# Kernel tuning notes

Hardware: AMD Instinct MI355X
Metric: run time of the kernel (lower is better)

## Reference

```python
import jax, jax.numpy as jnp
import numpy as np

B, NPG, D, E = 64, 1024, 128, 524288
N = B * NPG
K1, K2, K3 = 820, 656, 525  # ceil(0.8*1024), ceil(0.8*820), ceil(0.8*656)
VOCAB = 100000
EPS = 1e-5


def setup_inputs() -> dict:
    key = jax.random.key(0)
    ks = jax.random.split(key, 16)
    epg = E // B
    off = jnp.repeat(jnp.arange(B, dtype=jnp.int32) * NPG, epg)
    src = jax.random.randint(ks[0], (E,), 0, NPG, dtype=jnp.int32) + off
    dst = jax.random.randint(ks[1], (E,), 0, NPG, dtype=jnp.int32) + off
    edge_index = jnp.stack([src, dst])  # [2, E], within-graph edges
    node_idx = jax.random.randint(ks[2], (N, 1), 0, VOCAB, dtype=jnp.int32)
    def lin(k, o, i):
        return jax.random.normal(k, (o, i), jnp.float32) / np.sqrt(i).astype(np.float32)
    return dict(
        node_idx=node_idx, edge_index=edge_index,
        emb=jax.random.normal(ks[3], (VOCAB, D), jnp.float32),
        w1l=lin(ks[4], 128, D), b1l=jnp.zeros(128, jnp.float32), w1r=lin(ks[5], 128, D),
        pool_w=jax.random.normal(ks[6], (128,), jnp.float32) / np.float32(np.sqrt(128)),
        w2l=lin(ks[7], 128, 128), b2l=jnp.zeros(128, jnp.float32), w2r=lin(ks[8], 128, 128),
        fc1_w=lin(ks[9], 128, 256), fc1_b=jnp.zeros(128, jnp.float32),
        bn1_g=jnp.ones(128, jnp.float32), bn1_b=jnp.zeros(128, jnp.float32),
        fc2_w=lin(ks[10], 64, 128), fc2_b=jnp.zeros(64, jnp.float32),
        bn2_g=jnp.ones(64, jnp.float32), bn2_b=jnp.zeros(64, jnp.float32),
        lin_w=lin(ks[11], 1, 64), lin_b=jnp.zeros(1, jnp.float32),
    )


def _sage(x, src, dst, em, wl, bl, wr):
    # PyG SAGEConv: lin_l(mean_{j->i} x_j) + lin_r(x_i); em masks dropped edges
    n = x.shape[0]
    s = jax.ops.segment_sum(x[src] * em[:, None], dst, num_segments=n)
    c = jax.ops.segment_sum(em, dst, num_segments=n)
    mean = s / jnp.maximum(c, 1.0)[:, None]
    return mean @ wl.T + bl + x @ wr.T


def _topk(x, src, dst, em, w, k):
    # PyG TopKPooling: score = x.w/||w||, per-graph top-k, gate by tanh(score)
    n = x.shape[0]
    npg = n // B
    score = (x @ w) / jnp.linalg.norm(w)
    vals, idx = jax.lax.top_k(score.reshape(B, npg), k)  # [B,k]
    perm = (idx + (jnp.arange(B, dtype=idx.dtype) * npg)[:, None]).reshape(-1)
    xn = x[perm] * jnp.tanh(vals).reshape(-1)[:, None]
    new_id = jnp.full((n,), -1, jnp.int32).at[perm].set(jnp.arange(B * k, dtype=jnp.int32))
    ns, nd = new_id[src], new_id[dst]
    em2 = em * (ns >= 0) * (nd >= 0)  # keep only edges with both endpoints kept
    return xn, jnp.maximum(ns, 0), jnp.maximum(nd, 0), em2


def _readout(x, k):
    # global_max_pool || global_mean_pool (graphs are contiguous, size k)
    xr = x.reshape(B, k, -1)
    return jnp.concatenate([xr.max(axis=1), xr.mean(axis=1)], axis=1)


def _bn(x, g, b):
    m = x.mean(0)
    v = jnp.mean((x - m) ** 2, axis=0)  # biased var, as in BatchNorm1d training
    return (x - m) / jnp.sqrt(v + EPS) * g + b


def reference(node_idx, edge_index, emb, w1l, b1l, w1r, pool_w,
              w2l, b2l, w2r, fc1_w, fc1_b, bn1_g, bn1_b,
              fc2_w, fc2_b, bn2_g, bn2_b, lin_w, lin_b):
    src, dst = edge_index[0], edge_index[1]
    em = jnp.ones((E,), jnp.float32)
    x = emb[node_idx[:, 0]]                                   # [N,128]
    x = jax.nn.relu(_sage(x, src, dst, em, w1l, b1l, w1r))
    x, src, dst, em = _topk(x, src, dst, em, pool_w, K1)
    x1 = _readout(x, K1)
    x = jax.nn.relu(_sage(x, src, dst, em, w2l, b2l, w2r))
    x, src, dst, em = _topk(x, src, dst, em, pool_w, K2)
    x2 = _readout(x, K2)
    x = jax.nn.relu(_sage(x, src, dst, em, w2l, b2l, w2r))
    x, src, dst, em = _topk(x, src, dst, em, pool_w, K3)
    x3 = _readout(x, K3)
    h = x1 + x2 + x3                                          # [B,256]
    h = jax.nn.relu(_bn(h @ fc1_w.T + fc1_b, bn1_g, bn1_b))
    h = jax.nn.relu(_bn(h @ fc2_w.T + fc2_b, bn2_g, bn2_b))
    # dropout is identity in eval mode
    return jax.nn.sigmoid(h @ lin_w.T + lin_b)[:, 0]          # [B]
```

## Files before the change

### kernel.cpp

```cpp
#include <hip/hip_runtime.h>
#include <hip/hip_bf16.h>
#include <cstdint>
#include <cstddef>

#define NGRAPH 64
#define NPG0   1024
#define NNODE  65536
#define NEDGE  524288
#define EPG    8192
#define DIM    128
#define RCHUNK 16

typedef __attribute__((ext_vector_type(8))) short short8v;
typedef __attribute__((ext_vector_type(4))) float f32x4;

__device__ __forceinline__ unsigned bf16rne(float f) {
  unsigned u = __float_as_uint(f);
  return (u + 0x7FFFu + ((u >> 16) & 1u)) >> 16;
}

__global__ __launch_bounds__(256) void k_gather(const float* __restrict__ emb,
    const int* __restrict__ nid, float* __restrict__ x)
{
  int tid = blockIdx.x * 256 + threadIdx.x;
  int i = tid >> 5, lane = tid & 31;
  int row = nid[i];
  ((float4*)(x + (size_t)i * DIM))[lane] =
      ((const float4*)(emb + (size_t)row * DIM))[lane];
}

__global__ __launch_bounds__(64) void k_norm(const float* __restrict__ pw,
    float* __restrict__ inv_norm)
{
  int t = threadIdx.x;
  float a = pw[t], b = pw[t + 64];
  float v = a * a + b * b;
  for (int off = 32; off; off >>= 1) v += __shfl_xor(v, off);
  if (t == 0) *inv_norm = 1.0f / sqrtf(v);
}

__global__ __launch_bounds__(256) void k_prep_wfrag(
    const float* __restrict__ w1l, const float* __restrict__ w1r,
    const float* __restrict__ w2l, const float* __restrict__ w2r,
    short* __restrict__ whiF, short* __restrict__ wloF)
{
  int id = blockIdx.x * 256 + threadIdx.x;
  int set = id >> 15;
  int r = id & 32767;
  int j  = r & 7;
  int l  = (r >> 3) & 63;
  int nt = (r >> 9) & 7;
  int kk = r >> 12;
  int k = kk * 32 + ((l >> 4) & 3) * 8 + j;
  int n = nt * 16 + (l & 15);
  const float* wl = set ? w2l : w1l;
  const float* wr = set ? w2r : w1r;
  float w = (k < 128) ? wl[n * 128 + k] : wr[n * 128 + (k - 128)];
  unsigned hb = bf16rne(w);
  float hif = __uint_as_float(hb << 16);
  unsigned lb = bf16rne(w - hif);
  whiF[id] = (short)hb;
  wloF[id] = (short)lb;
}

__global__ __launch_bounds__(1024) void k_csr0(const int* __restrict__ ei,
    int* __restrict__ off_g, int* __restrict__ elist_g, float* __restrict__ c_out)
{
  __shared__ int cnt[1024];
  __shared__ int cur[1024];
  __shared__ int wsum[16];
  const int t = threadIdx.x, g = blockIdx.x;
  const int nodeBase = g * NPG0;
  const int e0 = g * EPG;
  cnt[t] = 0;
  __syncthreads();
  int sv8[8], dl8[8];
  #pragma unroll
  for (int i = 0; i < 8; ++i) {
    int e = e0 + t + i * 1024;
    sv8[i] = ei[e];
    dl8[i] = ei[NEDGE + e] - nodeBase;
    atomicAdd(&cnt[dl8[i]], 1);
  }
  __syncthreads();
  const int lane = t & 63, w = t >> 6;
  int cv = cnt[t];
  int x = cv;
  #pragma unroll
  for (int off = 1; off < 64; off <<= 1) {
    int y = __shfl_up(x, off);
    if (lane >= off) x += y;
  }
  if (lane == 63) wsum[w] = x;
  __syncthreads();
  if (t < 16) {
    int v = wsum[t];
    #pragma unroll
    for (int off2 = 1; off2 < 16; off2 <<= 1) {
      int y = __shfl_up(v, off2);
      if (t >= off2) v += y;
    }
    wsum[t] = v;
  }
  __syncthreads();
  int incl = x + (w ? wsum[w - 1] : 0);
  int excl = incl - cv;
  cur[t] = excl;
  int* offp = off_g + g * 1025;
  offp[t] = excl;
  if (t == 1023) offp[1024] = incl;
  c_out[nodeBase + t] = (float)cv;
  __syncthreads();
  int* elp = elist_g + g * EPG;
  #pragma unroll
  for (int i = 0; i < 8; ++i) {
    int pos = atomicAdd(&cur[dl8[i]], 1);
    elp[pos] = sv8[i];
  }
}

__global__ __launch_bounds__(256) void k_agg_gemm(
    const int* __restrict__ off_g, const int* __restrict__ elist_g,
    const float* __restrict__ x, float* __restrict__ h_out,
    const short* __restrict__ whiF, const short* __restrict__ wloF,
    const float* __restrict__ bl, const float* __restrict__ pw,
    float* __restrict__ score, int npg)
{
  __shared__ float sA[64 * 128];
  __shared__ float cntA[64];
  const int g     = blockIdx.x & 63;
  const int slice = blockIdx.x >> 6;
  const int nodeBase = g * npg;
  const int vbase = slice * 64;
  const int t = threadIdx.x;

  {
    const int gr = t >> 5, l32 = t & 31;
    const int* off = off_g + g * 1025;
    const int* el  = elist_g + g * EPG;
    #pragma unroll
    for (int i = 0; i < 8; ++i) {
      int vb = gr * 8 + i;
      int v = vbase + vb;
      float4 acc = {0.f, 0.f, 0.f, 0.f};
      int cn = 0;
      if (v < npg) {
        int e = off[v], end = off[v + 1];
        cn = end - e;
        for (; e + 4 <= end; e += 4) {
          int s0 = el[e], s1 = el[e + 1], s2 = el[e + 2], s3 = el[e + 3];
          float4 a0 = ((const float4*)(x + (size_t)s0 * DIM))[l32];
          float4 a1 = ((const float4*)(x + (size_t)s1 * DIM))[l32];
          float4 a2 = ((const float4*)(x + (size_t)s2 * DIM))[l32];
          float4 a3 = ((const float4*)(x + (size_t)s3 * DIM))[l32];
          acc.x += (a0.x + a1.x) + (a2.x + a3.x);
          acc.y += (a0.y + a1.y) + (a2.y + a3.y);
          acc.z += (a0.z + a1.z) + (a2.z + a3.z);
          acc.w += (a0.w + a1.w) + (a2.w + a3.w);
        }
        for (; e + 2 <= end; e += 2) {
          int s0 = el[e], s1 = el[e + 1];
          float4 a0 = ((const float4*)(x + (size_t)s0 * DIM))[l32];
          float4 a1 = ((const float4*)(x + (size_t)s1 * DIM))[l32];
          acc.x += a0.x + a1.x; acc.y += a0.y + a1.y;
          acc.z += a0.z + a1.z; acc.w += a0.w + a1.w;
        }
        if (e < end) {
          float4 a = ((const float4*)(x + (size_t)el[e] * DIM))[l32];
          acc.x += a.x; acc.y += a.y; acc.z += a.z; acc.w += a.w;
        }
      }
      ((float4*)(sA + vb * 128))[l32] = acc;
      if (l32 == 0) cntA[vb] = (float)cn;
    }
  }
  __syncthreads();

  const int wv = t >> 6, l = t & 63;
  const int lrow = l & 15, lk = l >> 4;
  const int rb = wv * 16;
  const int rowb = rb + lrow;
  const int rowg = nodeBase + min(vbase + rowb, npg - 1);
  const float invc = 1.0f / fmaxf(cntA[rowb], 1.0f);
  f32x4 acc[8];
  #pragma unroll
  for (int nt = 0; nt < 8; ++nt) acc[nt] = (f32x4){0.f, 0.f, 0.f, 0.f};
  const float* srow = sA + rowb * 128 + lk * 8;
  const float* xrow = x + (size_t)rowg * DIM + lk * 8;
  const short8v* bh = (const short8v*)whiF;
  const short8v* bo = (const short8v*)wloF;

  #pragma unroll
  for (int kk = 0; kk < 8; ++kk) {
    float av[8];
    if (kk < 4) {
      float4 a0 = *(const float4*)(srow + kk * 32);
      float4 a1 = *(const float4*)(srow + kk * 32 + 4);
      av[0] = a0.x * invc; av[1] = a0.y * invc;
      av[2] = a0.z * invc; av[3] = a0.w * invc;
      av[4] = a1.x * invc; av[5] = a1.y * invc;
      av[6] = a1.z * invc; av[7] = a1.w * invc;
    } else {
      float4 a0 = *(const float4*)(xrow + (kk - 4) * 32);
      float4 a1 = *(const float4*)(xrow + (kk - 4) * 32 + 4);
      av[0] = a0.x; av[1] = a0.y; av[2] = a0.z; av[3] = a0.w;
      av[4] = a1.x; av[5] = a1.y; av[6] = a1.z; av[7] = a1.w;
    }
    short8v ahi, alo;
    #pragma unroll
    for (int j = 0; j < 8; ++j) {
      unsigned hb = bf16rne(av[j]);
      float hif = __uint_as_float(hb << 16);
      ahi[j] = (short)hb;
      alo[j] = (short)bf16rne(av[j] - hif);
    }
    #pragma unroll
    for (int nt = 0; nt < 8; ++nt) {
      int fi = (kk * 8 + nt) * 64 + l;
      short8v bhi = bh[fi];
      short8v blo = bo[fi];
      acc[nt] = __builtin_amdgcn_mfma_f32_16x16x32_bf16(ahi, bhi, acc[nt], 0, 0, 0);
      acc[nt] = __builtin_amdgcn_mfma_f32_16x16x32_bf16(alo, bhi, acc[nt], 0, 0, 0);
      acc[nt] = __builtin_amdgcn_mfma_f32_16x16x32_bf16(ahi, blo, acc[nt], 0, 0, 0);
    }
  }

  float sp0 = 0.f, sp1 = 0.f, sp2 = 0.f, sp3 = 0.f;
  const int mbv = vbase + rb + lk * 4;
  #pragma unroll
  for (int nt = 0; nt < 8; ++nt) {
    int col = nt * 16 + lrow;
    float bb = bl[col], pv = pw[col];
    float h0 = fmaxf(acc[nt][0] + bb, 0.f);
    float h1 = fmaxf(acc[nt][1] + bb, 0.f);
    float h2 = fmaxf(acc[nt][2] + bb, 0.f);
    float h3 = fmaxf(acc[nt][3] + bb, 0.f);
    if (mbv + 0 < npg) h_out[(size_t)(nodeBase + mbv + 0) * DIM + col] = h0;
    if (mbv + 1 < npg) h_out[(size_t)(nodeBase + mbv + 1) * DIM + col] = h1;
    if (mbv + 2 < npg) h_out[(size_t)(nodeBase + mbv + 2) * DIM + col] = h2;
    if (mbv + 3 < npg) h_out[(size_t)(nodeBase + mbv + 3) * DIM + col] = h3;
    sp0 += h0 * pv; sp1 += h1 * pv; sp2 += h2 * pv; sp3 += h3 * pv;
  }
  #pragma unroll
  for (int off = 1; off <= 8; off <<= 1) {
    sp0 += __shfl_xor(sp0, off);
    sp1 += __shfl_xor(sp1, off);
    sp2 += __shfl_xor(sp2, off);
    sp3 += __shfl_xor(sp3, off);
  }
  if (lrow == 0) {
    if (mbv + 0 < npg) score[nodeBase + mbv + 0] = sp0;
    if (mbv + 1 < npg) score[nodeBase + mbv + 1] = sp1;
    if (mbv + 2 < npg) score[nodeBase + mbv + 2] = sp2;
    if (mbv + 3 < npg) score[nodeBase + mbv + 3] = sp3;
  }
}

__global__ __launch_bounds__(1024) void k_topk_fused(
    const float* __restrict__ score, const float* __restrict__ inv_norm_p,
    int npg, int k, int* __restrict__ sel_pos, float* __restrict__ sel_scale,
    int build_next, int write_eout,
    const int* __restrict__ ein_src, const int* __restrict__ ein_dst,
    int* __restrict__ eout_src, int* __restrict__ eout_dst,
    int* __restrict__ off_g, int* __restrict__ elist_g, float* __restrict__ c_out)
{
  __shared__ float key[1024];
  __shared__ int   idxs[1024];
  __shared__ int   nid[1024];
  __shared__ int   cnt[1024];
  __shared__ int   cur[1024];
  __shared__ int   wsum[16];
  const int t = threadIdx.x, g = blockIdx.x;
  const int base = g * npg;
  key[t] = (t < npg) ? score[base + t] : -3.402823466e38f;
  idxs[t] = t;
  nid[t] = -1;
  cnt[t] = 0;
  __syncthreads();
  for (int size = 2; size <= 1024; size <<= 1) {
    for (int stride = size >> 1; stride > 0; stride >>= 1) {
      int p = t ^ stride;
      if (p > t) {
        float ka = key[t], kb = key[p];
        int ia = idxs[t], ib = idxs[p];
        bool a_first = (ka > kb) || (ka == kb && ia < ib);
        bool desc = ((t & size) == 0);
        if (desc ? !a_first : a_first) {
          key[t] = kb; key[p] = ka; idxs[t] = ib; idxs[p] = ia;
        }
      }
      __syncthreads();
    }
  }
  if (t < k) {
    float inv = *inv_norm_p;
    int local = idxs[t];
    nid[local] = t;
    sel_pos[g * k + t] = base + local;
    sel_scale[g * k + t] = tanhf(key[t] * inv);
  }
  if (!build_next) return;
  __syncthreads();
  const int e0 = g * EPG;
  const int newBase = g * k;
  int lns[8], lnd[8];
  #pragma unroll
  for (int i = 0; i < 8; ++i) {
    int e = e0 + t + i * 1024;
    int sv = ein_src[e];
    int ns = -1, nd = -1;
    if (sv >= 0) {
      int dv = ein_dst[e];
      ns = nid[sv - base];
      nd = nid[dv - base];
      if (ns < 0 || nd < 0) ns = -1;
    }
    lns[i] = ns; lnd[i] = nd;
    if (write_eout) {
      eout_src[e] = (ns >= 0) ? (newBase + ns) : -1;
      eout_dst[e] = (ns >= 0) ? (newBase + nd) : -1;
    }
    if (ns >= 0) atomicAdd(&cnt[nd], 1);
  }
  __syncthreads();
  const int lane = t & 63, w = t >> 6;
  int cv = cnt[t];
  int x = cv;
  #pragma unroll
  for (int off = 1; off < 64; off <<= 1) {
    int y = __shfl_up(x, off);
    if (lane >= off) x += y;
  }
  if (lane == 63) wsum[w] = x;
  __syncthreads();
  if (t < 16) {
    int v = wsum[t];
    #pragma unroll
    for (int off2 = 1; off2 < 16; off2 <<= 1) {
      int y = __shfl_up(v, off2);
      if (t >= off2) v += y;
    }
    wsum[t] = v;
  }
  __syncthreads();
  int incl = x + (w ? wsum[w - 1] : 0);
  int excl = incl - cv;
  cur[t] = excl;
  off_g[g * 1025 + t] = excl;
  if (t < k) c_out[newBase + t] = (float)cv;
  __syncthreads();
  int* elp = elist_g + g * EPG;
  #pragma unroll
  for (int i = 0; i < 8; ++i) {
    if (lns[i] >= 0) {
      int pos = atomicAdd(&cur[lnd[i]], 1);
      elp[pos] = newBase + lns[i];
    }
  }
}

__global__ __launch_bounds__(256) void k_pool_part(const float* __restrict__ h,
    const int* __restrict__ sel_pos, const float* __restrict__ sel_scale, int k,
    float* __restrict__ xo, float* __restrict__ pmax, float* __restrict__ psum)
{
  __shared__ float4 smx[256], ssm[256];
  const int b  = blockIdx.x >> 4;
  const int ch = blockIdx.x & (RCHUNK - 1);
  const int rpc = (k + RCHUNK - 1) / RCHUNK;
  const int r0 = ch * rpc;
  const int r1 = min(k, r0 + rpc);
  const int d4  = threadIdx.x & 31;
  const int sub = threadIdx.x >> 5;
  const float NEG = -3.402823466e38f;
  float4 mx = {NEG, NEG, NEG, NEG};
  float4 sm = {0.f, 0.f, 0.f, 0.f};
  for (int r = r0 + sub; r < r1; r += 8) {
    int j = b * k + r;
    float scv = sel_scale[j];
    float4 v = ((const float4*)(h + (size_t)sel_pos[j] * DIM))[d4];
    v.x *= scv; v.y *= scv; v.z *= scv; v.w *= scv;
    ((float4*)(xo + (size_t)j * DIM))[d4] = v;
    mx.x = fmaxf(mx.x, v.x); mx.y = fmaxf(mx.y, v.y);
    mx.z = fmaxf(mx.z, v.z); mx.w = fmaxf(mx.w, v.w);
    sm.x += v.x; sm.y += v.y; sm.z += v.z; sm.w += v.w;
  }
  smx[threadIdx.x] = mx; ssm[threadIdx.x] = sm;
  __syncthreads();
  if (sub < 4) {
    #pragma unroll
    for (int step = 4; step >= 1; step >>= 1) {
      if (sub < step) {
        float4 m2 = smx[(sub + step) * 32 + d4];
        float4 s2 = ssm[(sub + step) * 32 + d4];
        mx = smx[sub * 32 + d4]; sm = ssm[sub * 32 + d4];
        mx.x = fmaxf(mx.x, m2.x); mx.y = fmaxf(mx.y, m2.y);
        mx.z = fmaxf(mx.z, m2.z); mx.w = fmaxf(mx.w, m2.w);
        sm.x += s2.x; sm.y += s2.y; sm.z += s2.z; sm.w += s2.w;
        smx[sub * 32 + d4] = mx; ssm[sub * 32 + d4] = sm;
      }
      __syncthreads();
    }
  }
  if (sub == 0) {
    int o = (b * RCHUNK + ch) * 32 + d4;
    ((float4*)pmax)[o] = smx[d4];
    ((float4*)psum)[o] = ssm[d4];
  }
}

__global__ __launch_bounds__(128) void k_readout_final(const float* __restrict__ pmax,
    const float* __restrict__ psum, int k, float* __restrict__ rdT, int add)
{
  int b = blockIdx.x, d = threadIdx.x;
  float mx = -3.402823466e38f, sm = 0.f;
  #pragma unroll
  for (int c = 0; c < RCHUNK; ++c) {
    int o = (b * RCHUNK + c) * 128 + d;
    mx = fmaxf(mx, pmax[o]);
    sm += psum[o];
  }
  float mean = sm / (float)k;
  int omx = d * 64 + b;
  int omn = (128 + d) * 64 + b;
  if (add) { rdT[omx] += mx; rdT[omn] += mean; }
  else     { rdT[omx]  = mx; rdT[omn]  = mean; }
}

__global__ __launch_bounds__(512) void k_mlp_fc1(const float* __restrict__ rdT,
    const float* __restrict__ fc1_w, const float* __restrict__ fc1_b,
    const float* __restrict__ g1, const float* __restrict__ be1,
    float* __restrict__ y1n)
{
  __shared__ float W[8 * 256];
  __shared__ float R[256 * 64];
  const int t = threadIdx.x, b = blockIdx.x;
  ((float4*)W)[t] = ((const float4*)(fc1_w + (size_t)b * 8 * 256))[t];
  #pragma unroll
  for (int i = 0; i < 8; ++i)
    ((float4*)R)[t + i * 512] = ((const float4*)rdT)[t + i * 512];
  __syncthreads();
  const int g = t & 63, w = t >> 6;
  const float* wrow = W + w * 256;
  float acc = 0.f;
  #pragma unroll 4
  for (int k = 0; k < 256; ++k) acc += R[k * 64 + g] * wrow[k];
  int f = b * 8 + w;
  float y = acc + fc1_b[f];
  float s = y, s2 = y * y;
  #pragma unroll
  for (int off = 32; off; off >>= 1) {
    s  += __shfl_xor(s,  off);
    s2 += __shfl_xor(s2, off);
  }
  float mu = s * 0.015625f;
  float var = s2 * 0.015625f - mu * mu;
  float inv = 1.0f / sqrtf(var + 1e-5f);
  y1n[f * 64 + g] = fmaxf((y - mu) * inv * g1[f] + be1[f], 0.f);
}

__global__ __launch_bounds__(1024) void k_mlp_rest(const float* __restrict__ y1n,
    const float* __restrict__ fc2_w, const float* __restrict__ fc2_b,
    const float* __restrict__ g2, const float* __restrict__ be2,
    const float* __restrict__ lin_w, const float* __restrict__ lin_b,
    float* __restrict__ out)
{
  __shared__ float W2[64 * 128];
  __shared__ float Y[128 * 64];
  __shared__ float part[16 * 64];
  const int t = threadIdx.x;
  #pragma unroll
  for (int i = 0; i < 2; ++i) {
    ((float4*)W2)[t + i * 1024] = ((const float4*)fc2_w)[t + i * 1024];
    ((float4*)Y) [t + i * 1024] = ((const float4*)y1n)[t + i * 1024];
  }
  __syncthreads();
  const int g = t & 63, w = t >> 6;
  float acc2[4] = {0.f, 0.f, 0.f, 0.f};
  const float* w20 = W2 + (w * 4 + 0) * 128;
  const float* w21 = W2 + (w * 4 + 1) * 128;
  const float* w22 = W2 + (w * 4 + 2) * 128;
  const float* w23 = W2 + (w * 4 + 3) * 128;
  #pragma unroll 4
  for (int k = 0; k < 128; ++k) {
    float yv = Y[k * 64 + g];
    acc2[0] += yv * w20[k];
    acc2[1] += yv * w21[k];
    acc2[2] += yv * w22[k];
    acc2[3] += yv * w23[k];
  }
  float pp = 0.f;
  #pragma unroll
  for (int j = 0; j < 4; ++j) {
    int m = w * 4 + j;
    float y = acc2[j] + fc2_b[m];
    float s = y, s2 = y * y;
    #pragma unroll
    for (int off = 32; off; off >>= 1) {
      s  += __shfl_xor(s,  off);
      s2 += __shfl_xor(s2, off);
    }
    float mu = s * 0.015625f;
    float var = s2 * 0.015625f - mu * mu;
    float inv = 1.0f / sqrtf(var + 1e-5f);
    float yn = fmaxf((y - mu) * inv * g2[m] + be2[m], 0.f);
    pp += yn * lin_w[m];
  }
  part[w * 64 + g] = pp;
  __syncthreads();
  if (w == 0) {
    float a = lin_b[0];
    #pragma unroll
    for (int c = 0; c < 16; ++c) a += part[c * 64 + g];
    out[g] = 1.0f / (1.0f + expf(-a));
  }
}

extern "C" void kernel_launch(void* const* d_in, const int* in_sizes, int n_in,
                              void* d_out, int out_size, void* d_ws, size_t ws_size,
                              hipStream_t stream) {
  const int*   node_idx = (const int*)  d_in[0];
  const int*   edge_idx = (const int*)  d_in[1];
  const float* emb      = (const float*)d_in[2];
  const float* w1l      = (const float*)d_in[3];
  const float* b1l      = (const float*)d_in[4];
  const float* w1r      = (const float*)d_in[5];
  const float* pool_w   = (const float*)d_in[6];
  const float* w2l      = (const float*)d_in[7];
  const float* b2l      = (const float*)d_in[8];
  const float* w2r      = (const float*)d_in[9];
  const float* fc1_w    = (const float*)d_in[10];
  const float* fc1_b    = (const float*)d_in[11];
  const float* bn1_g    = (const float*)d_in[12];
  const float* bn1_b    = (const float*)d_in[13];
  const float* fc2_w    = (const float*)d_in[14];
  const float* fc2_b    = (const float*)d_in[15];
  const float* bn2_g    = (const float*)d_in[16];
  const float* bn2_b    = (const float*)d_in[17];
  const float* lin_w    = (const float*)d_in[18];
  const float* lin_b    = (const float*)d_in[19];
  float* out = (float*)d_out;

  char* p = (char*)d_ws;
  auto alloc = [&](size_t bytes) -> void* {
    void* r = (void*)p;
    p += (bytes + 255) & ~(size_t)255;
    return r;
  };
  float* x_cur     = (float*)alloc((size_t)NNODE * DIM * 4);
  float* s_buf     = (float*)alloc((size_t)NNODE * DIM * 4);
  float* c_buf     = (float*)alloc((size_t)NNODE * 4);
  float* score     = (float*)alloc((size_t)NNODE * 4);
  int*   sel_pos   = (int*)  alloc((size_t)NGRAPH * 820 * 4);
  float* sel_scale = (float*)alloc((size_t)NGRAPH * 820 * 4);
  int*   src_cur   = (int*)  alloc((size_t)NEDGE * 4);
  int*   dst_cur   = (int*)  alloc((size_t)NEDGE * 4);
  int*   off_g     = (int*)  alloc((size_t)NGRAPH * 1025 * 4);
  int*   elist_g   = (int*)  alloc((size_t)NGRAPH * EPG * 4);
  float* rdT       = (float*)alloc((size_t)256 * 64 * 4);
  short* whiF      = (short*)alloc((size_t)2 * 32768 * 2);
  short* wloF      = (short*)alloc((size_t)2 * 32768 * 2);
  float* y1n       = (float*)alloc((size_t)128 * 64 * 4);
  float* pmax      = (float*)alloc((size_t)NGRAPH * RCHUNK * 128 * 4);
  float* psum      = (float*)alloc((size_t)NGRAPH * RCHUNK * 128 * 4);
  float* inv_norm  = (float*)alloc(256);

  k_gather<<<NNODE * 32 / 256, 256, 0, stream>>>(emb, node_idx, x_cur);
  k_norm<<<1, 64, 0, stream>>>(pool_w, inv_norm);
  k_prep_wfrag<<<256, 256, 0, stream>>>(w1l, w1r, w2l, w2r, whiF, wloF);
  k_csr0<<<NGRAPH, 1024, 0, stream>>>(edge_idx, off_g, elist_g, c_buf);

  const int Ks[3] = {820, 656, 525};
  int npg = NPG0;
  for (int stage = 0; stage < 3; ++stage) {
    const short* whi_s = whiF + (stage ? 32768 : 0);
    const short* wlo_s = wloF + (stage ? 32768 : 0);
    const float* bl    = stage ? b2l : b1l;
    int k = Ks[stage];
    int slices = (npg + 63) >> 6;

    k_agg_gemm<<<slices * 64, 256, 0, stream>>>(off_g, elist_g, x_cur, s_buf,
                                                whi_s, wlo_s, bl, pool_w,
                                                score, npg);
    const int* ein_s = (stage == 0) ? edge_idx          : src_cur;
    const int* ein_d = (stage == 0) ? (edge_idx + NEDGE) : dst_cur;
    k_topk_fused<<<NGRAPH, 1024, 0, stream>>>(score, inv_norm, npg, k,
        sel_pos, sel_scale,
        (stage < 2) ? 1 : 0, (stage == 0) ? 1 : 0,
        ein_s, ein_d, src_cur, dst_cur,
        off_g, elist_g, c_buf);
    k_pool_part<<<NGRAPH * RCHUNK, 256, 0, stream>>>(s_buf, sel_pos, sel_scale, k,
                                                     x_cur, pmax, psum);
    k_readout_final<<<NGRAPH, 128, 0, stream>>>(pmax, psum, k, rdT, stage == 0 ? 0 : 1);
    npg = k;
  }

  k_mlp_fc1<<<16, 512, 0, stream>>>(rdT, fc1_w, fc1_b, bn1_g, bn1_b, y1n);
  k_mlp_rest<<<1, 1024, 0, stream>>>(y1n, fc2_w, fc2_b, bn2_g, bn2_b,
                                     lin_w, lin_b, out);
}
```

Measured before the change: 277.3 us.

## Pair-row gather aggregation, register/shuffle bitonic sort, merged readout finalization

The aggregation phase now walks two destination rows together, so each thread has eight independent neighbor-row loads in flight instead of four, and it stores the sums to shared memory with an XOR swizzle to reduce bank conflicts. The per-graph top-k bitonic sort keeps keys in registers and uses wavefront shuffles for strides below 64. Shared memory and barriers are used only for larger strides. The three per-stage readout-finalize launches are replaced by one launch after the loop, which needs three partial-result buffers. The trade-off is more register pressure in the aggregation kernel and two barriers per large-stride step.

Measured after the change: 265.5 us. 4.3% less time.

```diff
diff --git a/kernel.cpp b/kernel.cpp
--- a/kernel.cpp
+++ b/kernel.cpp
@@ -10,6 +10,7 @@
 #define EPG    8192
 #define DIM    128
 #define RCHUNK 16
+#define PSTRIDE ((size_t)NGRAPH * RCHUNK * 128)
 
 typedef __attribute__((ext_vector_type(8))) short short8v;
 typedef __attribute__((ext_vector_type(4))) float f32x4;
@@ -17,6 +18,26 @@
 __device__ __forceinline__ unsigned bf16rne(float f) {
   unsigned u = __float_as_uint(f);
   return (u + 0x7FFFu + ((u >> 16) & 1u)) >> 16;
+}
+
+__device__ __forceinline__ void drain_row(const int* __restrict__ el,
+    const float* __restrict__ x, int l32, int e, int end, float4& acc)
+{
+  for (; e + 4 <= end; e += 4) {
+    int s0 = el[e], s1 = el[e+1], s2 = el[e+2], s3 = el[e+3];
+    float4 a0 = ((const float4*)(x + (size_t)s0 * DIM))[l32];
+    float4 a1 = ((const float4*)(x + (size_t)s1 * DIM))[l32];
+    float4 a2 = ((const float4*)(x + (size_t)s2 * DIM))[l32];
+    float4 a3 = ((const float4*)(x + (size_t)s3 * DIM))[l32];
+    acc.x += (a0.x + a1.x) + (a2.x + a3.x);
+    acc.y += (a0.y + a1.y) + (a2.y + a3.y);
+    acc.z += (a0.z + a1.z) + (a2.z + a3.z);
+    acc.w += (a0.w + a1.w) + (a2.w + a3.w);
+  }
+  for (; e < end; ++e) {
+    float4 a = ((const float4*)(x + (size_t)el[e] * DIM))[l32];
+    acc.x += a.x; acc.y += a.y; acc.z += a.z; acc.w += a.w;
+  }
 }
 
 __global__ __launch_bounds__(256) void k_gather(const float* __restrict__ emb,
@@ -133,45 +154,47 @@
   const int nodeBase = g * npg;
   const int vbase = slice * 64;
   const int t = threadIdx.x;
+  float4* sA4 = (float4*)sA;
 
   {
     const int gr = t >> 5, l32 = t & 31;
     const int* off = off_g + g * 1025;
     const int* el  = elist_g + g * EPG;
     #pragma unroll
-    for (int i = 0; i < 8; ++i) {
-      int vb = gr * 8 + i;
-      int v = vbase + vb;
-      float4 acc = {0.f, 0.f, 0.f, 0.f};
-      int cn = 0;
-      if (v < npg) {
-        int e = off[v], end = off[v + 1];
-        cn = end - e;
-        for (; e + 4 <= end; e += 4) {
-          int s0 = el[e], s1 = el[e + 1], s2 = el[e + 2], s3 = el[e + 3];
-          float4 a0 = ((const float4*)(x + (size_t)s0 * DIM))[l32];
-          float4 a1 = ((const float4*)(x + (size_t)s1 * DIM))[l32];
-          float4 a2 = ((const float4*)(x + (size_t)s2 * DIM))[l32];
-          float4 a3 = ((const float4*)(x + (size_t)s3 * DIM))[l32];
-          acc.x += (a0.x + a1.x) + (a2.x + a3.x);
-          acc.y += (a0.y + a1.y) + (a2.y + a3.y);
-          acc.z += (a0.z + a1.z) + (a2.z + a3.z);
-          acc.w += (a0.w + a1.w) + (a2.w + a3.w);
-        }
-        for (; e + 2 <= end; e += 2) {
-          int s0 = el[e], s1 = el[e + 1];
-          float4 a0 = ((const float4*)(x + (size_t)s0 * DIM))[l32];
-          float4 a1 = ((const float4*)(x + (size_t)s1 * DIM))[l32];
-          acc.x += a0.x + a1.x; acc.y += a0.y + a1.y;
-          acc.z += a0.z + a1.z; acc.w += a0.w + a1.w;
-        }
-        if (e < end) {
-          float4 a = ((const float4*)(x + (size_t)el[e] * DIM))[l32];
-          acc.x += a.x; acc.y += a.y; acc.z += a.z; acc.w += a.w;
-        }
+    for (int ip = 0; ip < 4; ++ip) {
+      const int vbA = gr * 8 + ip * 2, vbB = vbA + 1;
+      const int vA = vbase + vbA, vB = vbase + vbB;
+      float4 accA = {0.f,0.f,0.f,0.f}, accB = {0.f,0.f,0.f,0.f};
+      int eA = 0, endA = 0, eB = 0, endB = 0;
+      if (vA < npg) { eA = off[vA]; endA = off[vA + 1]; }
+      if (vB < npg) { eB = off[vB]; endB = off[vB + 1]; }
+      const int cnA = endA - eA, cnB = endB - eB;
+      while (eA + 4 <= endA && eB + 4 <= endB) {
+        int a0 = el[eA], a1 = el[eA+1], a2 = el[eA+2], a3 = el[eA+3];
+        int b0 = el[eB], b1 = el[eB+1], b2 = el[eB+2], b3 = el[eB+3];
+        float4 xa0 = ((const float4*)(x + (size_t)a0 * DIM))[l32];
+        float4 xa1 = ((const float4*)(x + (size_t)a1 * DIM))[l32];
+        float4 xa2 = ((const float4*)(x + (size_t)a2 * DIM))[l32];
+        float4 xa3 = ((const float4*)(x + (size_t)a3 * DIM))[l32];
+        float4 xb0 = ((const float4*)(x + (size_t)b0 * DIM))[l32];
+        float4 xb1 = ((const float4*)(x + (size_t)b1 * DIM))[l32];
+        float4 xb2 = ((const float4*)(x + (size_t)b2 * DIM))[l32];
+        float4 xb3 = ((const float4*)(x + (size_t)b3 * DIM))[l32];
+        accA.x += (xa0.x + xa1.x) + (xa2.x + xa3.x);
+        accA.y += (xa0.y + xa1.y) + (xa2.y + xa3.y);
+        accA.z += (xa0.z + xa1.z) + (xa2.z + xa3.z);
+        accA.w += (xa0.w + xa1.w) + (xa2.w + xa3.w);
+        accB.x += (xb0.x + xb1.x) + (xb2.x + xb3.x);
+        accB.y += (xb0.y + xb1.y) + (xb2.y + xb3.y);
+        accB.z += (xb0.z + xb1.z) + (xb2.z + xb3.z);
+        accB.w += (xb0.w + xb1.w) + (xb2.w + xb3.w);
+        eA += 4; eB += 4;
       }
-      ((float4*)(sA + vb * 128))[l32] = acc;
-      if (l32 == 0) cntA[vb] = (float)cn;
+      drain_row(el, x, l32, eA, endA, accA);
+      drain_row(el, x, l32, eB, endB, accB);
+      sA4[vbA * 32 + (l32 ^ (vbA & 7))] = accA;
+      sA4[vbB * 32 + (l32 ^ (vbB & 7))] = accB;
+      if (l32 == 0) { cntA[vbA] = (float)cnA; cntA[vbB] = (float)cnB; }
     }
   }
   __syncthreads();
@@ -180,12 +203,13 @@
   const int lrow = l & 15, lk = l >> 4;
   const int rb = wv * 16;
   const int rowb = rb + lrow;
+  const int rsw = rowb & 7;
   const int rowg = nodeBase + min(vbase + rowb, npg - 1);
   const float invc = 1.0f / fmaxf(cntA[rowb], 1.0f);
   f32x4 acc[8];
   #pragma unroll
   for (int nt = 0; nt < 8; ++nt) acc[nt] = (f32x4){0.f, 0.f, 0.f, 0.f};
-  const float* srow = sA + rowb * 128 + lk * 8;
+  const float4* sArow = sA4 + rowb * 32;
   const float* xrow = x + (size_t)rowg * DIM + lk * 8;
   const short8v* bh = (const short8v*)whiF;
   const short8v* bo = (const short8v*)wloF;
@@ -194,8 +218,9 @@
   for (int kk = 0; kk < 8; ++kk) {
     float av[8];
     if (kk < 4) {
-      float4 a0 = *(const float4*)(srow + kk * 32);
-      float4 a1 = *(const float4*)(srow + kk * 32 + 4);
+      int sbase = kk * 8 + lk * 2;
+      float4 a0 = sArow[(sbase + 0) ^ rsw];
+      float4 a1 = sArow[(sbase + 1) ^ rsw];
       av[0] = a0.x * invc; av[1] = a0.y * invc;
       av[2] = a0.z * invc; av[3] = a0.w * invc;
       av[4] = a1.x * invc; av[5] = a1.y * invc;
@@ -272,32 +297,41 @@
   __shared__ int   wsum[16];
   const int t = threadIdx.x, g = blockIdx.x;
   const int base = g * npg;
-  key[t] = (t < npg) ? score[base + t] : -3.402823466e38f;
-  idxs[t] = t;
+  float rk = (t < npg) ? score[base + t] : -3.402823466e38f;
+  int   ri = t;
   nid[t] = -1;
   cnt[t] = 0;
-  __syncthreads();
+
+  #pragma unroll
   for (int size = 2; size <= 1024; size <<= 1) {
-    for (int stride = size >> 1; stride > 0; stride >>= 1) {
-      int p = t ^ stride;
-      if (p > t) {
-        float ka = key[t], kb = key[p];
-        int ia = idxs[t], ib = idxs[p];
-        bool a_first = (ka > kb) || (ka == kb && ia < ib);
-        bool desc = ((t & size) == 0);
-        if (desc ? !a_first : a_first) {
-          key[t] = kb; key[p] = ka; idxs[t] = ib; idxs[p] = ia;
-        }
-      }
+    for (int stride = size >> 1; stride >= 64; stride >>= 1) {
+      key[t] = rk; idxs[t] = ri;
       __syncthreads();
-    }
-  }
+      float km = key[t ^ stride];
+      int   im = idxs[t ^ stride];
+      __syncthreads();
+      bool mf = (rk > km) || (rk == km && ri < im);
+      bool desc = ((t & size) == 0);
+      bool lower = ((t & stride) == 0);
+      bool keep = desc ? (lower ? mf : !mf) : (lower ? !mf : mf);
+      if (!keep) { rk = km; ri = im; }
+    }
+    for (int stride = (size >> 1) > 32 ? 32 : (size >> 1); stride >= 1; stride >>= 1) {
+      float km = __shfl_xor(rk, stride);
+      int   im = __shfl_xor(ri, stride);
+      bool mf = (rk > km) || (rk == km && ri < im);
+      bool desc = ((t & size) == 0);
+      bool lower = ((t & stride) == 0);
+      bool keep = desc ? (lower ? mf : !mf) : (lower ? !mf : mf);
+      if (!keep) { rk = km; ri = im; }
+    }
+  }
+
   if (t < k) {
     float inv = *inv_norm_p;
-    int local = idxs[t];
-    nid[local] = t;
-    sel_pos[g * k + t] = base + local;
-    sel_scale[g * k + t] = tanhf(key[t] * inv);
+    nid[ri] = t;
+    sel_pos[g * k + t] = base + ri;
+    sel_scale[g * k + t] = tanhf(rk * inv);
   }
   if (!build_next) return;
   __syncthreads();
@@ -408,22 +442,29 @@
   }
 }
 
-__global__ __launch_bounds__(128) void k_readout_final(const float* __restrict__ pmax,
-    const float* __restrict__ psum, int k, float* __restrict__ rdT, int add)
+__global__ __launch_bounds__(128) void k_readout_final3(
+    const float* __restrict__ pmax, const float* __restrict__ psum,
+    int k0, int k1, int k2, float* __restrict__ rdT)
 {
   int b = blockIdx.x, d = threadIdx.x;
-  float mx = -3.402823466e38f, sm = 0.f;
-  #pragma unroll
-  for (int c = 0; c < RCHUNK; ++c) {
-    int o = (b * RCHUNK + c) * 128 + d;
-    mx = fmaxf(mx, pmax[o]);
-    sm += psum[o];
-  }
-  float mean = sm / (float)k;
-  int omx = d * 64 + b;
-  int omn = (128 + d) * 64 + b;
-  if (add) { rdT[omx] += mx; rdT[omn] += mean; }
-  else     { rdT[omx]  = mx; rdT[omn]  = mean; }
+  const int ks[3] = {k0, k1, k2};
+  float tmx = 0.f, tmn = 0.f;
+  #pragma unroll
+  for (int s = 0; s < 3; ++s) {
+    const float* pm = pmax + (size_t)s * PSTRIDE;
+    const float* ps = psum + (size_t)s * PSTRIDE;
+    float mx = -3.402823466e38f, sm = 0.f;
+    #pragma unroll
+    for (int c = 0; c < RCHUNK; ++c) {
+      int o = (b * RCHUNK + c) * 128 + d;
+      mx = fmaxf(mx, pm[o]);
+      sm += ps[o];
+    }
+    tmx += mx;
+    tmn += sm / (float)ks[s];
+  }
+  rdT[d * 64 + b] = tmx;
+  rdT[(128 + d) * 64 + b] = tmn;
 }
 
 __global__ __launch_bounds__(512) void k_mlp_fc1(const float* __restrict__ rdT,
@@ -560,8 +601,8 @@
   short* whiF      = (short*)alloc((size_t)2 * 32768 * 2);
   short* wloF      = (short*)alloc((size_t)2 * 32768 * 2);
   float* y1n       = (float*)alloc((size_t)128 * 64 * 4);
-  float* pmax      = (float*)alloc((size_t)NGRAPH * RCHUNK * 128 * 4);
-  float* psum      = (float*)alloc((size_t)NGRAPH * RCHUNK * 128 * 4);
+  float* pmax      = (float*)alloc(PSTRIDE * 3 * 4);
+  float* psum      = (float*)alloc(PSTRIDE * 3 * 4);
   float* inv_norm  = (float*)alloc(256);
 
   k_gather<<<NNODE * 32 / 256, 256, 0, stream>>>(emb, node_idx, x_cur);
@@ -589,11 +630,11 @@
         ein_s, ein_d, src_cur, dst_cur,
         off_g, elist_g, c_buf);
     k_pool_part<<<NGRAPH * RCHUNK, 256, 0, stream>>>(s_buf, sel_pos, sel_scale, k,
-                                                     x_cur, pmax, psum);
-    k_readout_final<<<NGRAPH, 128, 0, stream>>>(pmax, psum, k, rdT, stage == 0 ? 0 : 1);
+        x_cur, pmax + (size_t)stage * PSTRIDE, psum + (size_t)stage * PSTRIDE);
     npg = k;
   }
 
+  k_readout_final3<<<NGRAPH, 128, 0, stream>>>(pmax, psum, Ks[0], Ks[1], Ks[2], rdT);
   k_mlp_fc1<<<16, 512, 0, stream>>>(rdT, fc1_w, fc1_b, bn1_g, bn1_b, y1n);
   k_mlp_rest<<<1, 1024, 0, stream>>>(y1n, fc2_w, fc2_b, bn2_g, bn2_b,
                                      lin_w, lin_b, out);
```
